# Performance work log

Measured on AMD Instinct MI355X. Metric: run time of the kernel, lower is better.

## Reference

```python
import jax, jax.numpy as jnp
import numpy as np

EMPTY_IDX = 6  # relabeling of the original -1 ('EMPTY') expert to row 6 of the stacked tables


def setup_inputs() -> dict:
    key = jax.random.key(0)
    k1, k2, k3, k4, k5, k6 = jax.random.split(key, 6)
    B, L, H, T, E = 32, 2048, 768, 12, 7
    return {
        "sequence_output": jax.random.normal(k1, (B, L, H), dtype=jnp.float32),
        "module_net_w": jax.random.normal(k2, (E, H, H), dtype=jnp.float32),
        "span_net_w": jax.random.normal(k3, (E, H, 2), dtype=jnp.float32),
        "turns": jax.random.randint(k4, (B, T, 2), 0, L),
        "key_phrase_span": jax.random.randint(k5, (B, T, 2), 0, L),
        "module_index": jax.random.randint(k6, (B, T), 0, E),
    }


def reference(sequence_output, module_net_w, span_net_w, turns, key_phrase_span, module_index):
    seq = sequence_output            # [B, L, H]
    B, L, H = seq.shape
    T = turns.shape[1]
    f32 = seq.dtype

    eidx = module_index              # [B, T], 0..6 (6 == EMPTY, original -1)
    mod_mask = (eidx != EMPTY_IDX).astype(f32)            # module_index != -1
    start_pos = turns[:, :, 0]       # [B, T] turn start token positions
    turns_mask = (start_pos >= 0).astype(f32)             # turns[:,:,0] != -1

    # context_hidden_step = sequence_output[arange(B), start] for every step
    ctx = jnp.take_along_axis(seq, start_pos[:, :, None], axis=1)   # [B, T, H]

    # einsum('bh,bhz,blz->blz'): (ctx @ W_expert) broadcast-multiplied with seq.
    # Compute ctx @ W for ALL experts (tables are tiny), then gather per (b, t).
    cW_all = jnp.einsum('bth,ehz->btez', ctx, module_net_w)         # [B, T, 7, H]
    gidx = jnp.broadcast_to(eidx[:, :, None, None], (B, T, 1, H))
    cW = jnp.take_along_axis(cW_all, gidx, axis=2).squeeze(2)       # [B, T, H]

    span_w = span_net_w[eidx]        # [B, T, H, 2] per-sample expert span weights
    # logits[b,t,l,k] = sum_z seq[b,l,z] * cW[b,t,z] * span_w[b,t,z,k]
    v = cW[..., None] * span_w                                      # [B, T, H, 2]
    logits = jnp.einsum('blz,btzk->btlk', seq, v)                   # [B, T, L, 2]

    # CrossEntropyLoss(ignore_index=-1, reduction='none') over the L axis
    logsm = jax.nn.log_softmax(logits, axis=2)                      # [B, T, L, 2]
    tgt = key_phrase_span[:, :, :T][:, :T]  # [B, T, 2]
    tgt = key_phrase_span
    safe = jnp.clip(tgt, 0, L - 1)                                  # [B, T, 2]
    picked = jnp.take_along_axis(logsm, safe[:, :, None, :], axis=2).squeeze(2)  # [B, T, 2]
    ce = jnp.where(tgt >= 0, -picked, jnp.zeros((), f32))           # [B, T, 2]
    step_loss = 0.5 * (ce[..., 0] + ce[..., 1]) * mod_mask          # [B, T]

    loss = (step_loss * turns_mask).sum() / turns_mask.sum()
    return loss
```

## Files before the change

### kernel.cpp

```cpp
#include <hip/hip_runtime.h>
#include <math.h>

#define Bz 32
#define Lz 2048
#define Hz 768
#define Tz 12
#define Ez 7
#define EMPTYIDX 6
#define NCOL 24
#define LCHUNK 128
#define NCHUNK 16

__global__ void k0_compact(const int* __restrict__ midx,
                           int* __restrict__ off, int* __restrict__ items) {
    __shared__ int cnt[Ez];
    __shared__ int offs[Ez + 1];
    int tid = threadIdx.x;
    if (tid < Ez) cnt[tid] = 0;
    __syncthreads();
    int e = midx[tid];
    e = min(max(e, 0), Ez - 1);
    int r = atomicAdd(&cnt[e], 1);
    __syncthreads();
    if (tid == 0) {
        int acc = 0;
        for (int j = 0; j < Ez; ++j) { offs[j] = acc; acc += cnt[j]; }
        offs[Ez] = acc;
    }
    __syncthreads();
    items[offs[e] + r] = tid;
    if (tid <= Ez) off[tid] = offs[tid];
}

#define K1A_ZC 3
#define K1A_HB 48
#define K1A_HC 16
__global__ void k1a_cw(const float* __restrict__ seq, const float* __restrict__ W,
                       const int* __restrict__ turns,
                       const int* __restrict__ off, const int* __restrict__ items,
                       float* __restrict__ cW) {
    int bx = blockIdx.x;
    int e  = bx % Ez;
    int zc = (bx / Ez) % K1A_ZC;
    int hc = bx / (Ez * K1A_ZC);
    int z  = zc * 256 + threadIdx.x;
    int h0 = hc * K1A_HB;
    int off0 = off[e];
    int cnt  = off[e + 1] - off0;
    const float* Wb = W + ((size_t)e * Hz + h0) * Hz + z;
    float w[K1A_HB];
#pragma unroll
    for (int j = 0; j < K1A_HB; ++j) w[j] = Wb[(size_t)j * Hz];

    for (int n = 0; n < cnt; ++n) {
        int i  = items[off0 + n];
        int b  = i / Tz;
        int st = turns[2 * i];
        st = min(max(st, 0), Lz - 1);
        const float* c = seq + ((size_t)(b * Lz + st)) * Hz + h0;
        float acc = 0.f;
#pragma unroll
        for (int j = 0; j < K1A_HB; ++j) acc = fmaf(c[j], w[j], acc);
        atomicAdd(&cW[(size_t)i * Hz + z], acc);
    }
}

__global__ void k1b_v(const float* __restrict__ cW, const float* __restrict__ spanw,
                      const int* __restrict__ midx, float* __restrict__ v) {
    int idx = blockIdx.x * 256 + threadIdx.x;
    int i = idx / Hz;
    int z = idx - i * Hz;
    int e = midx[i];
    e = min(max(e, 0), Ez - 1);
    float cw = cW[idx];
    int b = i / Tz, t = i - b * Tz;
    size_t vb = ((size_t)(b * NCOL + t * 2)) * Hz + z;
    v[vb]      = cw * spanw[(e * Hz + z) * 2 + 0];
    v[vb + Hz] = cw * spanw[(e * Hz + z) * 2 + 1];
}

#define BK 64
#define ATS (BK + 4)
__global__ void k2_logits(const float* __restrict__ seq, const float* __restrict__ v,
                          float* __restrict__ pm, float* __restrict__ ps) {
    int bx = blockIdx.x;
    int b  = bx / NCHUNK;
    int ch = bx % NCHUNK;
    int l0 = ch * LCHUNK;
    int tid = threadIdx.x;
    int rg = tid >> 3;
    int cg = tid & 7;
    __shared__ float at[LCHUNK][ATS];
    __shared__ float vt[NCOL][ATS];
    __shared__ float red_m[NCOL][33];
    __shared__ float red_s[NCOL][33];
    float acc[4][3];
#pragma unroll
    for (int r = 0; r < 4; ++r)
#pragma unroll
        for (int j = 0; j < 3; ++j) acc[r][j] = 0.f;

    const float* A = seq + ((size_t)b * Lz + l0) * Hz;
    const float* V = v + (size_t)b * NCOL * Hz;

    for (int k0 = 0; k0 < Hz; k0 += BK) {
#pragma unroll
        for (int p = 0; p < 8; ++p) {
            int j  = tid + p * 256;
            int r  = j >> 4, c4 = j & 15;
            float4 x = *(const float4*)&A[(size_t)r * Hz + k0 + c4 * 4];
            *(float4*)&at[r][c4 * 4] = x;
        }
        {
            int j = tid;
            int c = j >> 4, q = j & 15;
            *(float4*)&vt[c][q * 4] = *(const float4*)&V[(size_t)c * Hz + k0 + q * 4];
            if (tid < 128) {
                j = tid + 256; c = j >> 4; q = j & 15;
                *(float4*)&vt[c][q * 4] = *(const float4*)&V[(size_t)c * Hz + k0 + q * 4];
            }
        }
        __syncthreads();
#pragma unroll
        for (int kk = 0; kk < BK; kk += 4) {
            float4 a0 = *(const float4*)&at[rg +  0][kk];
            float4 a1 = *(const float4*)&at[rg + 32][kk];
            float4 a2 = *(const float4*)&at[rg + 64][kk];
            float4 a3 = *(const float4*)&at[rg + 96][kk];
            float4 v0 = *(const float4*)&vt[cg * 3 + 0][kk];
            float4 v1 = *(const float4*)&vt[cg * 3 + 1][kk];
            float4 v2 = *(const float4*)&vt[cg * 3 + 2][kk];
#define DOT(ACC, AV, VV) ACC = fmaf(AV.w, VV.w, fmaf(AV.z, VV.z, fmaf(AV.y, VV.y, fmaf(AV.x, VV.x, ACC))))
            DOT(acc[0][0], a0, v0); DOT(acc[0][1], a0, v1); DOT(acc[0][2], a0, v2);
            DOT(acc[1][0], a1, v0); DOT(acc[1][1], a1, v1); DOT(acc[1][2], a1, v2);
            DOT(acc[2][0], a2, v0); DOT(acc[2][1], a2, v1); DOT(acc[2][2], a2, v2);
            DOT(acc[3][0], a3, v0); DOT(acc[3][1], a3, v1); DOT(acc[3][2], a3, v2);
#undef DOT
        }
        __syncthreads();
    }
#pragma unroll
    for (int j = 0; j < 3; ++j) {
        int c = cg * 3 + j;
        float m = fmaxf(fmaxf(acc[0][j], acc[1][j]), fmaxf(acc[2][j], acc[3][j]));
        float s = expf(acc[0][j] - m) + expf(acc[1][j] - m) +
                  expf(acc[2][j] - m) + expf(acc[3][j] - m);
        red_m[c][rg] = m;
        red_s[c][rg] = s;
    }
    __syncthreads();
    if (tid < NCOL) {
        int c = tid;
        float m = red_m[c][0];
        for (int r = 1; r < 32; ++r) m = fmaxf(m, red_m[c][r]);
        float s = 0.f;
        for (int r = 0; r < 32; ++r) s += red_s[c][r] * expf(red_m[c][r] - m);
        pm[((size_t)b * NCOL + c) * NCHUNK + ch] = m;
        ps[((size_t)b * NCOL + c) * NCHUNK + ch] = s;
    }
}

__global__ void k3_picked(const float* __restrict__ seq, const float* __restrict__ v,
                          const int* __restrict__ kps, float* __restrict__ picked) {
    int i = blockIdx.x;
    int b = i / Tz, t = i % Tz;
    int lane = threadIdx.x;
    for (int k = 0; k < 2; ++k) {
        int tgt  = kps[2 * i + k];
        int safe = min(max(tgt, 0), Lz - 1);
        const float* srow = seq + ((size_t)b * Lz + safe) * Hz;
        const float* vcol = v + ((size_t)(b * NCOL + t * 2 + k)) * Hz;
        float sum = 0.f;
#pragma unroll
        for (int q = 0; q < Hz / 64; ++q) {
            int z = lane + q * 64;
            sum = fmaf(srow[z], vcol[z], sum);
        }
        for (int o = 32; o > 0; o >>= 1) sum += __shfl_down(sum, o, 64);
        if (lane == 0) picked[b * NCOL + t * 2 + k] = sum;
    }
}

__global__ void k4_final(const int* __restrict__ midx, const int* __restrict__ turns,
                         const int* __restrict__ kps,
                         const float* __restrict__ pm, const float* __restrict__ ps,
                         const float* __restrict__ picked, float* __restrict__ out) {
    int tid = threadIdx.x;
    int i = tid;
    int b = i / Tz, t = i % Tz;
    int e = midx[i];
    float modm  = (e != EMPTYIDX) ? 1.f : 0.f;
    float tmask = (turns[2 * i] >= 0) ? 1.f : 0.f;
    float ce[2];
#pragma unroll
    for (int k = 0; k < 2; ++k) {
        int c = t * 2 + k;
        const float* pmr = pm + ((size_t)b * NCOL + c) * NCHUNK;
        const float* psr = ps + ((size_t)b * NCOL + c) * NCHUNK;
        float m = pmr[0];
        for (int chn = 1; chn < NCHUNK; ++chn) m = fmaxf(m, pmr[chn]);
        float s = 0.f;
        for (int chn = 0; chn < NCHUNK; ++chn) s += psr[chn] * expf(pmr[chn] - m);
        float lse = m + logf(s);
        int tgt = kps[2 * i + k];
        ce[k] = (tgt >= 0) ? (lse - picked[b * NCOL + c]) : 0.f;
    }
    float contrib = 0.5f * (ce[0] + ce[1]) * modm * tmask;

    __shared__ float wsum[6], wmask[6];
    float sl = contrib, sm = tmask;
    for (int o = 32; o > 0; o >>= 1) {
        sl += __shfl_down(sl, o, 64);
        sm += __shfl_down(sm, o, 64);
    }
    int w = tid >> 6, lane = tid & 63;
    if (lane == 0) { wsum[w] = sl; wmask[w] = sm; }
    __syncthreads();
    if (tid == 0) {
        float a = 0.f, mk = 0.f;
        for (int ww = 0; ww < 6; ++ww) { a += wsum[ww]; mk += wmask[ww]; }
        out[0] = a / mk;
    }
}

extern "C" void kernel_launch(void* const* d_in, const int* in_sizes, int n_in,
                              void* d_out, int out_size, void* d_ws, size_t ws_size,
                              hipStream_t stream) {
    const float* seq   = (const float*)d_in[0];
    const float* W     = (const float*)d_in[1];
    const float* spanw = (const float*)d_in[2];
    const int*   turns = (const int*)d_in[3];
    const int*   kps   = (const int*)d_in[4];
    const int*   midx  = (const int*)d_in[5];
    float* out = (float*)d_out;

    char* ws = (char*)d_ws;
    int*   off    = (int*)(ws + 0);
    int*   items  = (int*)(ws + 64);
    float* cW     = (float*)(ws + 2048);
    float* v      = (float*)(ws + 2048 + 1179648);
    float* pm     = (float*)(ws + 2048 + 1179648 + 2359296);
    float* ps     = (float*)(ws + 2048 + 1179648 + 2359296 + 49152);
    float* picked = (float*)(ws + 2048 + 1179648 + 2359296 + 98304);

    hipMemsetAsync(cW, 0, (size_t)384 * Hz * sizeof(float), stream);
    hipLaunchKernelGGL(k0_compact, dim3(1), dim3(Bz * Tz), 0, stream, midx, off, items);
    hipLaunchKernelGGL(k1a_cw, dim3(Ez * K1A_ZC * K1A_HC), dim3(256), 0, stream,
                       seq, W, turns, off, items, cW);
    hipLaunchKernelGGL(k1b_v, dim3((384 * Hz) / 256), dim3(256), 0, stream,
                       cW, spanw, midx, v);
    hipLaunchKernelGGL(k2_logits, dim3(Bz * NCHUNK), dim3(256), 0, stream, seq, v, pm, ps);
    hipLaunchKernelGGL(k3_picked, dim3(Bz * Tz), dim3(64), 0, stream, seq, v, kps, picked);
    hipLaunchKernelGGL(k4_final, dim3(1), dim3(Bz * Tz), 0, stream,
                       midx, turns, kps, pm, ps, picked, out);
}
```

Before: 369.8 us.

## Restructure logits GEMM with register prefetch, fuse picked gather, drop atomics

The first-stage reduction no longer uses atomicAdd into a zeroed cW buffer. It writes per-h-chunk partials that k1b_v sums, which removes the memset and the atomics at the cost of a larger workspace. The logits kernel changes so each thread owns one row and half the K slice. It keeps 24 column accumulators, reads v directly from global/L1, prefetches the next seq tile into registers, and uses an XOR-swizzled LDS tile. Picked logits are now captured inside this kernel, so the separate k3 launch goes away. The risks are higher register pressure and uncoalesced per-thread v reads.

```diff
diff --git a/kernel.cpp b/kernel.cpp
--- a/kernel.cpp
+++ b/kernel.cpp
@@ -8,6 +8,7 @@
 #define Ez 7
 #define EMPTYIDX 6
 #define NCOL 24
+#define NITEM (Bz * Tz)
 #define LCHUNK 128
 #define NCHUNK 16
 
@@ -38,7 +39,7 @@
 __global__ void k1a_cw(const float* __restrict__ seq, const float* __restrict__ W,
                        const int* __restrict__ turns,
                        const int* __restrict__ off, const int* __restrict__ items,
-                       float* __restrict__ cW) {
+                       float* __restrict__ pc) {
     int bx = blockIdx.x;
     int e  = bx % Ez;
     int zc = (bx / Ez) % K1A_ZC;
@@ -61,123 +62,136 @@
         float acc = 0.f;
 #pragma unroll
         for (int j = 0; j < K1A_HB; ++j) acc = fmaf(c[j], w[j], acc);
-        atomicAdd(&cW[(size_t)i * Hz + z], acc);
-    }
-}
-
-__global__ void k1b_v(const float* __restrict__ cW, const float* __restrict__ spanw,
+        pc[((size_t)hc * NITEM + i) * Hz + z] = acc;
+    }
+}
+
+__global__ void k1b_v(const float* __restrict__ pc, const float* __restrict__ spanw,
                       const int* __restrict__ midx, float* __restrict__ v) {
     int idx = blockIdx.x * 256 + threadIdx.x;
     int i = idx / Hz;
     int z = idx - i * Hz;
+    float cw = 0.f;
+#pragma unroll
+    for (int hc = 0; hc < K1A_HC; ++hc)
+        cw += pc[((size_t)hc * NITEM + i) * Hz + z];
     int e = midx[i];
     e = min(max(e, 0), Ez - 1);
-    float cw = cW[idx];
     int b = i / Tz, t = i - b * Tz;
     size_t vb = ((size_t)(b * NCOL + t * 2)) * Hz + z;
     v[vb]      = cw * spanw[(e * Hz + z) * 2 + 0];
     v[vb + Hz] = cw * spanw[(e * Hz + z) * 2 + 1];
 }
 
-#define BK 64
-#define ATS (BK + 4)
-__global__ void k2_logits(const float* __restrict__ seq, const float* __restrict__ v,
-                          float* __restrict__ pm, float* __restrict__ ps) {
-    int bx = blockIdx.x;
-    int b  = bx / NCHUNK;
-    int ch = bx % NCHUNK;
-    int l0 = ch * LCHUNK;
+#define BKP 64
+#define NPH (Hz / BKP)
+__global__ __launch_bounds__(256, 2)
+void k2_logits(const float* __restrict__ seq, const float* __restrict__ v,
+               const int* __restrict__ kps,
+               float* __restrict__ pm, float* __restrict__ ps,
+               float* __restrict__ picked) {
+    int bx  = blockIdx.x;
+    int b   = bx / NCHUNK;
+    int ch  = bx % NCHUNK;
+    int l0  = ch * LCHUNK;
     int tid = threadIdx.x;
-    int rg = tid >> 3;
-    int cg = tid & 7;
-    __shared__ float at[LCHUNK][ATS];
-    __shared__ float vt[NCOL][ATS];
-    __shared__ float red_m[NCOL][33];
-    __shared__ float red_s[NCOL][33];
-    float acc[4][3];
-#pragma unroll
-    for (int r = 0; r < 4; ++r)
-#pragma unroll
-        for (int j = 0; j < 3; ++j) acc[r][j] = 0.f;
+    int r   = tid & (LCHUNK - 1);
+    int kh  = __builtin_amdgcn_readfirstlane(tid >> 7);
+
+    __shared__ float at[LCHUNK][BKP];
+    __shared__ float lg[LCHUNK][NCOL + 1];
+    __shared__ float redm[NCOL][4], reds[NCOL][4];
+    __shared__ int   ksafe[NCOL];
+
+    if (tid < NCOL) {
+        int t0 = kps[b * NCOL + tid];
+        ksafe[tid] = min(max(t0, 0), Lz - 1);
+    }
+
+    float acc[NCOL];
+#pragma unroll
+    for (int c = 0; c < NCOL; ++c) acc[c] = 0.f;
 
     const float* A = seq + ((size_t)b * Lz + l0) * Hz;
     const float* V = v + (size_t)b * NCOL * Hz;
 
-    for (int k0 = 0; k0 < Hz; k0 += BK) {
+    float4 g[8];
+#pragma unroll
+    for (int p = 0; p < 8; ++p) {
+        int j = tid + p * 256, rr = j >> 4, c4 = j & 15;
+        g[p] = *(const float4*)&A[(size_t)rr * Hz + c4 * 4];
+    }
+
+    for (int ph = 0; ph < NPH; ++ph) {
+        __syncthreads();
 #pragma unroll
         for (int p = 0; p < 8; ++p) {
-            int j  = tid + p * 256;
-            int r  = j >> 4, c4 = j & 15;
-            float4 x = *(const float4*)&A[(size_t)r * Hz + k0 + c4 * 4];
-            *(float4*)&at[r][c4 * 4] = x;
-        }
-        {
-            int j = tid;
-            int c = j >> 4, q = j & 15;
-            *(float4*)&vt[c][q * 4] = *(const float4*)&V[(size_t)c * Hz + k0 + q * 4];
-            if (tid < 128) {
-                j = tid + 256; c = j >> 4; q = j & 15;
-                *(float4*)&vt[c][q * 4] = *(const float4*)&V[(size_t)c * Hz + k0 + q * 4];
+            int j = tid + p * 256, rr = j >> 4, c4 = j & 15;
+            *(float4*)&at[rr][((c4 ^ (rr & 15)) << 2)] = g[p];
+        }
+        __syncthreads();
+        if (ph + 1 < NPH) {
+#pragma unroll
+            for (int p = 0; p < 8; ++p) {
+                int j = tid + p * 256, rr = j >> 4, c4 = j & 15;
+                g[p] = *(const float4*)&A[(size_t)rr * Hz + (ph + 1) * BKP + c4 * 4];
             }
         }
-        __syncthreads();
-#pragma unroll
-        for (int kk = 0; kk < BK; kk += 4) {
-            float4 a0 = *(const float4*)&at[rg +  0][kk];
-            float4 a1 = *(const float4*)&at[rg + 32][kk];
-            float4 a2 = *(const float4*)&at[rg + 64][kk];
-            float4 a3 = *(const float4*)&at[rg + 96][kk];
-            float4 v0 = *(const float4*)&vt[cg * 3 + 0][kk];
-            float4 v1 = *(const float4*)&vt[cg * 3 + 1][kk];
-            float4 v2 = *(const float4*)&vt[cg * 3 + 2][kk];
-#define DOT(ACC, AV, VV) ACC = fmaf(AV.w, VV.w, fmaf(AV.z, VV.z, fmaf(AV.y, VV.y, fmaf(AV.x, VV.x, ACC))))
-            DOT(acc[0][0], a0, v0); DOT(acc[0][1], a0, v1); DOT(acc[0][2], a0, v2);
-            DOT(acc[1][0], a1, v0); DOT(acc[1][1], a1, v1); DOT(acc[1][2], a1, v2);
-            DOT(acc[2][0], a2, v0); DOT(acc[2][1], a2, v1); DOT(acc[2][2], a2, v2);
-            DOT(acc[3][0], a3, v0); DOT(acc[3][1], a3, v1); DOT(acc[3][2], a3, v2);
-#undef DOT
-        }
-        __syncthreads();
-    }
-#pragma unroll
-    for (int j = 0; j < 3; ++j) {
-        int c = cg * 3 + j;
-        float m = fmaxf(fmaxf(acc[0][j], acc[1][j]), fmaxf(acc[2][j], acc[3][j]));
-        float s = expf(acc[0][j] - m) + expf(acc[1][j] - m) +
-                  expf(acc[2][j] - m) + expf(acc[3][j] - m);
-        red_m[c][rg] = m;
-        red_s[c][rg] = s;
+        float a[32];
+#pragma unroll
+        for (int q4 = 0; q4 < 8; ++q4) {
+            int c4 = kh * 8 + q4;
+            float4 x = *(const float4*)&at[r][((c4 ^ (r & 15)) << 2)];
+            a[q4 * 4 + 0] = x.x; a[q4 * 4 + 1] = x.y;
+            a[q4 * 4 + 2] = x.z; a[q4 * 4 + 3] = x.w;
+        }
+        const float* Vp = V + ph * BKP + kh * 32;
+#pragma unroll 2
+        for (int c = 0; c < NCOL; ++c) {
+            const float* vp = Vp + (size_t)c * Hz;
+            float s0 = 0.f, s1 = 0.f;
+#pragma unroll
+            for (int q = 0; q < 32; q += 2) {
+                s0 = fmaf(a[q],     vp[q],     s0);
+                s1 = fmaf(a[q + 1], vp[q + 1], s1);
+            }
+            acc[c] += s0 + s1;
+        }
+    }
+
+    if (kh == 1) {
+#pragma unroll
+        for (int c = 0; c < NCOL; ++c) lg[r][c] = acc[c];
+    }
+    __syncthreads();
+    if (kh == 0) {
+#pragma unroll
+        for (int c = 0; c < NCOL; ++c) { acc[c] += lg[r][c]; lg[r][c] = acc[c]; }
+        int grow = l0 + r;
+#pragma unroll
+        for (int c = 0; c < NCOL; ++c)
+            if (ksafe[c] == grow) picked[b * NCOL + c] = acc[c];
+    }
+    __syncthreads();
+
+    if (tid < 96) {
+        int c = tid >> 2, rg = tid & 3;
+        float m = lg[rg * 32][c];
+        for (int rr = rg * 32 + 1; rr < rg * 32 + 32; ++rr)
+            m = fmaxf(m, lg[rr][c]);
+        float s = 0.f;
+        for (int rr = rg * 32; rr < rg * 32 + 32; ++rr)
+            s += expf(lg[rr][c] - m);
+        redm[c][rg] = m; reds[c][rg] = s;
     }
     __syncthreads();
     if (tid < NCOL) {
-        int c = tid;
-        float m = red_m[c][0];
-        for (int r = 1; r < 32; ++r) m = fmaxf(m, red_m[c][r]);
+        float m = redm[tid][0];
+        for (int j = 1; j < 4; ++j) m = fmaxf(m, redm[tid][j]);
         float s = 0.f;
-        for (int r = 0; r < 32; ++r) s += red_s[c][r] * expf(red_m[c][r] - m);
-        pm[((size_t)b * NCOL + c) * NCHUNK + ch] = m;
-        ps[((size_t)b * NCOL + c) * NCHUNK + ch] = s;
-    }
-}
-
-__global__ void k3_picked(const float* __restrict__ seq, const float* __restrict__ v,
-                          const int* __restrict__ kps, float* __restrict__ picked) {
-    int i = blockIdx.x;
-    int b = i / Tz, t = i % Tz;
-    int lane = threadIdx.x;
-    for (int k = 0; k < 2; ++k) {
-        int tgt  = kps[2 * i + k];
-        int safe = min(max(tgt, 0), Lz - 1);
-        const float* srow = seq + ((size_t)b * Lz + safe) * Hz;
-        const float* vcol = v + ((size_t)(b * NCOL + t * 2 + k)) * Hz;
-        float sum = 0.f;
-#pragma unroll
-        for (int q = 0; q < Hz / 64; ++q) {
-            int z = lane + q * 64;
-            sum = fmaf(srow[z], vcol[z], sum);
-        }
-        for (int o = 32; o > 0; o >>= 1) sum += __shfl_down(sum, o, 64);
-        if (lane == 0) picked[b * NCOL + t * 2 + k] = sum;
+        for (int j = 0; j < 4; ++j) s += reds[tid][j] * expf(redm[tid][j] - m);
+        pm[((size_t)b * NCOL + tid) * NCHUNK + ch] = m;
+        ps[((size_t)b * NCOL + tid) * NCHUNK + ch] = s;
     }
 }
 
@@ -236,21 +250,20 @@
 
     char* ws = (char*)d_ws;
     int*   off    = (int*)(ws + 0);
-    int*   items  = (int*)(ws + 64);
-    float* cW     = (float*)(ws + 2048);
-    float* v      = (float*)(ws + 2048 + 1179648);
-    float* pm     = (float*)(ws + 2048 + 1179648 + 2359296);
-    float* ps     = (float*)(ws + 2048 + 1179648 + 2359296 + 49152);
-    float* picked = (float*)(ws + 2048 + 1179648 + 2359296 + 98304);
-
-    hipMemsetAsync(cW, 0, (size_t)384 * Hz * sizeof(float), stream);
-    hipLaunchKernelGGL(k0_compact, dim3(1), dim3(Bz * Tz), 0, stream, midx, off, items);
+    int*   items  = (int*)(ws + 256);
+    float* pc     = (float*)(ws + 2048);
+    float* v      = (float*)(ws + 2048 + 18874368);
+    float* pm     = (float*)(ws + 2048 + 18874368 + 2359296);
+    float* ps     = (float*)(ws + 2048 + 18874368 + 2359296 + 49152);
+    float* picked = (float*)(ws + 2048 + 18874368 + 2359296 + 98304);
+
+    hipLaunchKernelGGL(k0_compact, dim3(1), dim3(NITEM), 0, stream, midx, off, items);
     hipLaunchKernelGGL(k1a_cw, dim3(Ez * K1A_ZC * K1A_HC), dim3(256), 0, stream,
-                       seq, W, turns, off, items, cW);
-    hipLaunchKernelGGL(k1b_v, dim3((384 * Hz) / 256), dim3(256), 0, stream,
-                       cW, spanw, midx, v);
-    hipLaunchKernelGGL(k2_logits, dim3(Bz * NCHUNK), dim3(256), 0, stream, seq, v, pm, ps);
-    hipLaunchKernelGGL(k3_picked, dim3(Bz * Tz), dim3(64), 0, stream, seq, v, kps, picked);
-    hipLaunchKernelGGL(k4_final, dim3(1), dim3(Bz * Tz), 0, stream,
+                       seq, W, turns, off, items, pc);
+    hipLaunchKernelGGL(k1b_v, dim3((NITEM * Hz) / 256), dim3(256), 0, stream,
+                       pc, spanw, midx, v);
+    hipLaunchKernelGGL(k2_logits, dim3(Bz * NCHUNK), dim3(256), 0, stream,
+                       seq, v, kps, pm, ps, picked);
+    hipLaunchKernelGGL(k4_final, dim3(1), dim3(NITEM), 0, stream,
                        midx, turns, kps, pm, ps, picked, out);
 }
```

Result: slower. 439.3 us (+18.8%).
